# Performance work log

Measured on AMD Instinct MI355X. Metric: run time of the kernel, lower is better.

The kernel has to match this reference:

```python
import jax, jax.numpy as jnp
import numpy as np

T = 524288
INPUT_LEN = 64
N_MEMORY = 64
OUTPUT_LEN = 32


def setup_inputs() -> dict:
    key = jax.random.key(0)
    k_x, k_w1, k_b1, k_w2, k_b2 = jax.random.split(key, 5)
    s = 0.05  # tf.random_normal_initializer default stddev
    return {
        "inputs": jax.random.normal(k_x, (T, INPUT_LEN), dtype=jnp.float32),
        "W1": s * jax.random.normal(k_w1, (INPUT_LEN, 2 * N_MEMORY), dtype=jnp.float32),
        "B1": s * jax.random.normal(k_b1, (1, 2 * N_MEMORY), dtype=jnp.float32),
        "W2": s * jax.random.normal(k_w2, (N_MEMORY, OUTPUT_LEN), dtype=jnp.float32),
        "B2": s * jax.random.normal(k_b2, (1, OUTPUT_LEN), dtype=jnp.float32),
    }


def reference(inputs, W1, B1, W2, B2):
    n_memory = W2.shape[0]
    # gates: h = sigmoid(x W1 + B1), split into left/right halves  [T, M] each
    h = jax.nn.sigmoid(inputs @ W1 + B1)
    left, right = jnp.split(h, 2, axis=1)
    prod = left * right
    # affine linear recurrence: u_t = prod_{t-1} * u_{t-1} + (1 - left_{t-1}), u_0 = 0
    a = prod[:-1]            # [T-1, M] multiplicative coeffs
    b = 1.0 - left[:-1]      # [T-1, M] additive terms

    def step(u, ab):
        a_t, b_t = ab
        u = a_t * u + b_t
        return u, u

    u0 = jnp.zeros((n_memory,), dtype=inputs.dtype)
    _, us = jax.lax.scan(step, u0, (a, b))
    z = jnp.concatenate([u0[None, :], us], axis=0)  # [T, M]
    out = z @ W2 + B2                               # [T, output_len]
    return out
```

## Files before the change

kernel.cpp:

```cpp
#include <hip/hip_runtime.h>

#define TT    524288
#define CHUNK 512
#define NCH   (TT / CHUNK)
#define SUB   64
#define NSUB  (CHUNK / SUB)

typedef __attribute__((ext_vector_type(8))) short short8;
typedef __attribute__((ext_vector_type(4))) float f32x4;

__device__ __forceinline__ unsigned short f2bf(float f) {
    union { float f; unsigned u; } v; v.f = f;
    unsigned r = v.u + 0x7FFFu + ((v.u >> 16) & 1u);
    return (unsigned short)(r >> 16);
}
__device__ __forceinline__ unsigned packbf2(float a, float b) {
    union { float f; unsigned u; } va, vb; va.f = a; vb.f = b;
    unsigned ra = va.u + 0x7FFFu + ((va.u >> 16) & 1u);
    unsigned rb = vb.u + 0x7FFFu + ((vb.u >> 16) & 1u);
    return (ra >> 16) | (rb & 0xFFFF0000u);
}
__device__ __forceinline__ float2 unpackbf2(unsigned w) {
    union { unsigned u; float f; } a, b;
    a.u = w << 16; b.u = w & 0xFFFF0000u;
    return make_float2(a.f, b.f);
}
__device__ __forceinline__ float sigf(float v) {
    return __builtin_amdgcn_rcpf(1.0f + __expf(-v));
}

template <bool EMIT>
__global__ __launch_bounds__(256, 3)
void dphase(const float* __restrict__ x, const float* __restrict__ W1,
            const float* __restrict__ B1, const float* __restrict__ W2,
            const float* __restrict__ B2, const float* __restrict__ carry,
            float* __restrict__ Aout, float* __restrict__ Bout,
            float* __restrict__ out)
{
    __shared__ __align__(16) short    W1t[128 * 72];
    __shared__ float    B1s[128];
    __shared__ __align__(16) short    XZ[SUB * 72];
    __shared__ unsigned abp[SUB * 65];
    __shared__ float    segA[4 * 66], segB[4 * 66];
    __shared__ float    ucur[64];
    __shared__ __align__(16) short    W2t[32 * 72];
    __shared__ float    B2s[32];

    const int tid  = threadIdx.x;
    const int c    = blockIdx.x;
    const int wave = tid >> 6;
    const int lane = tid & 63;
    const int quad = lane >> 4;
    const int lr   = lane & 15;

    for (int i = tid; i < 2048; i += 256) {
        float4 w4 = ((const float4*)W1)[i];
        int k = i >> 5, n0 = (i & 31) * 4;
        W1t[(n0 + 0) * 72 + k] = (short)f2bf(w4.x);
        W1t[(n0 + 1) * 72 + k] = (short)f2bf(w4.y);
        W1t[(n0 + 2) * 72 + k] = (short)f2bf(w4.z);
        W1t[(n0 + 3) * 72 + k] = (short)f2bf(w4.w);
    }
    if (tid < 128) B1s[tid] = B1[tid];
    if (EMIT) {
        for (int i = tid; i < 512; i += 256) {
            float4 w4 = ((const float4*)W2)[i];
            int k = i >> 3, n0 = (i & 7) * 4;
            W2t[(n0 + 0) * 72 + k] = (short)f2bf(w4.x);
            W2t[(n0 + 1) * 72 + k] = (short)f2bf(w4.y);
            W2t[(n0 + 2) * 72 + k] = (short)f2bf(w4.z);
            W2t[(n0 + 3) * 72 + k] = (short)f2bf(w4.w);
        }
        if (tid < 32) B2s[tid] = B2[tid];
        if (tid < 64) ucur[tid] = carry[c * 64 + tid];
    }

    const float4* xg = (const float4*)(x + (size_t)c * CHUNK * 64);
    float4 xr0 = xg[tid], xr1 = xg[tid + 256], xr2 = xg[tid + 512], xr3 = xg[tid + 768];

    float sA = 1.0f, sB = 0.0f;

    for (int s = 0; s < NSUB; ++s) {
        {
            float4 v; int f;
#define PUTX(R, J) { v = (R); f = tid + 256 * (J); int row = f >> 4, c4 = (f & 15) * 4; \
            unsigned lo = (unsigned)f2bf(v.x) | ((unsigned)f2bf(v.y) << 16); \
            unsigned hi = (unsigned)f2bf(v.z) | ((unsigned)f2bf(v.w) << 16); \
            *(uint2*)&XZ[row * 72 + c4] = make_uint2(lo, hi); }
            PUTX(xr0, 0) PUTX(xr1, 1) PUTX(xr2, 2) PUTX(xr3, 3)
#undef PUTX
        }
        __syncthreads();

        if (s + 1 < NSUB) {
            const float4* xn = xg + (size_t)(s + 1) * 1024;
            xr0 = xn[tid]; xr1 = xn[tid + 256]; xr2 = xn[tid + 512]; xr3 = xn[tid + 768];
        }

        f32x4 acc[8];
        #pragma unroll
        for (int j = 0; j < 8; ++j) {
            float b = B1s[j * 16 + lr];
            acc[j][0] = b; acc[j][1] = b; acc[j][2] = b; acc[j][3] = b;
        }
        const short8 a0 = *(const short8*)&XZ[(wave * 16 + lr) * 72 + quad * 8];
        const short8 a1 = *(const short8*)&XZ[(wave * 16 + lr) * 72 + quad * 8 + 32];
        #pragma unroll
        for (int j = 0; j < 8; ++j) {
            const short8 b0 = *(const short8*)&W1t[(j * 16 + lr) * 72 + quad * 8];
            const short8 b1 = *(const short8*)&W1t[(j * 16 + lr) * 72 + quad * 8 + 32];
            acc[j] = __builtin_amdgcn_mfma_f32_16x16x32_bf16(a0, b0, acc[j], 0, 0, 0);
            acc[j] = __builtin_amdgcn_mfma_f32_16x16x32_bf16(a1, b1, acc[j], 0, 0, 0);
        }

        #pragma unroll
        for (int j = 0; j < 4; ++j) {
            #pragma unroll
            for (int r = 0; r < 4; ++r) {
                float hl = sigf(acc[j][r]);
                float hr = sigf(acc[j + 4][r]);
                int m = wave * 16 + quad * 4 + r;
                abp[m * 65 + j * 16 + lr] = packbf2(hl * hr, 1.0f - hl);
            }
        }
        __syncthreads();

        float A = 1.0f, Bv = 0.0f;
        #pragma unroll
        for (int t = 0; t < 16; ++t) {
            float2 f2 = unpackbf2(abp[(wave * 16 + t) * 65 + lane]);
            Bv = fmaf(f2.x, Bv, f2.y); A *= f2.x;
        }
        segA[wave * 66 + lane] = A;
        segB[wave * 66 + lane] = Bv;
        __syncthreads();

        if (EMIT) {
            float u = ucur[lane];
            #pragma unroll
            for (int q = 0; q < 3; ++q)
                if (q < wave) u = fmaf(segA[q * 66 + lane], u, segB[q * 66 + lane]);
            #pragma unroll
            for (int t = 0; t < 16; ++t) {
                float2 f2 = unpackbf2(abp[(wave * 16 + t) * 65 + lane]);
                XZ[(wave * 16 + t) * 72 + lane] = (short)f2bf(u);
                u = fmaf(f2.x, u, f2.y);
            }
            if (wave == 3) ucur[lane] = u;

            const short8 za0 = *(const short8*)&XZ[(wave * 16 + lr) * 72 + quad * 8];
            const short8 za1 = *(const short8*)&XZ[(wave * 16 + lr) * 72 + quad * 8 + 32];
            const size_t row0g = (size_t)c * CHUNK + (size_t)s * SUB;
            #pragma unroll
            for (int nt = 0; nt < 2; ++nt) {
                f32x4 cc;
                float b = B2s[nt * 16 + lr];
                cc[0] = b; cc[1] = b; cc[2] = b; cc[3] = b;
                const short8 b0 = *(const short8*)&W2t[(nt * 16 + lr) * 72 + quad * 8];
                const short8 b1 = *(const short8*)&W2t[(nt * 16 + lr) * 72 + quad * 8 + 32];
                cc = __builtin_amdgcn_mfma_f32_16x16x32_bf16(za0, b0, cc, 0, 0, 0);
                cc = __builtin_amdgcn_mfma_f32_16x16x32_bf16(za1, b1, cc, 0, 0, 0);
                #pragma unroll
                for (int r = 0; r < 4; ++r) {
                    int m = wave * 16 + quad * 4 + r;
                    out[(row0g + m) * 32 + nt * 16 + lr] = cc[r];
                }
            }
            __syncthreads();
        } else {
            if (tid < 64) {
                #pragma unroll
                for (int q = 0; q < 4; ++q) {
                    float A2 = segA[q * 66 + tid], B2v = segB[q * 66 + tid];
                    sB = fmaf(A2, sB, B2v); sA *= A2;
                }
            }
        }
    }

    if (!EMIT && tid < 64) { Aout[c * 64 + tid] = sA; Bout[c * 64 + tid] = sB; }
}

__global__ void carry_scan(const float* __restrict__ Aar, const float* __restrict__ Bar,
                           float* __restrict__ carry)
{
    __shared__ float sA[16 * 66], sB[16 * 66];
    const int tid = threadIdx.x;
    const int ch = tid & 63, seg = tid >> 6;
    const int c0 = seg * (NCH / 16);

    float A = 1.0f, B = 0.0f;
    #pragma unroll 8
    for (int i = 0; i < NCH / 16; ++i) {
        const int idx = c0 + i;
        const float a = Aar[idx * 64 + ch];
        const float b = Bar[idx * 64 + ch];
        B = fmaf(a, B, b); A *= a;
    }
    sA[seg * 66 + ch] = A;
    sB[seg * 66 + ch] = B;
    __syncthreads();

    float u = 0.0f;
    #pragma unroll
    for (int q = 0; q < 15; ++q)
        if (q < seg) u = fmaf(sA[q * 66 + ch], u, sB[q * 66 + ch]);
    #pragma unroll 8
    for (int i = 0; i < NCH / 16; ++i) {
        const int idx = c0 + i;
        carry[idx * 64 + ch] = u;
        u = fmaf(Aar[idx * 64 + ch], u, Bar[idx * 64 + ch]);
    }
}

extern "C" void kernel_launch(void* const* d_in, const int* in_sizes, int n_in,
                              void* d_out, int out_size, void* d_ws, size_t ws_size,
                              hipStream_t stream)
{
    const float* x  = (const float*)d_in[0];
    const float* W1 = (const float*)d_in[1];
    const float* B1 = (const float*)d_in[2];
    const float* W2 = (const float*)d_in[3];
    const float* B2 = (const float*)d_in[4];
    float* out = (float*)d_out;

    float* Aar   = (float*)d_ws;
    float* Bar   = Aar + NCH * 64;
    float* carry = Bar + NCH * 64;

    dphase<false><<<NCH, 256, 0, stream>>>(x, W1, B1, W2, B2, nullptr,
                                           Aar, Bar, nullptr);
    carry_scan<<<1, 1024, 0, stream>>>(Aar, Bar, carry);
    dphase<true><<<NCH, 256, 0, stream>>>(x, W1, B1, W2, B2, carry,
                                          nullptr, nullptr, out);
}
```

Baseline: 301.7 us.

## Store gate coefficients in phase one and drop recompute in emit phase

```diff
diff --git a/kernel.cpp b/kernel.cpp
--- a/kernel.cpp
+++ b/kernel.cpp
@@ -29,22 +29,17 @@
     return __builtin_amdgcn_rcpf(1.0f + __expf(-v));
 }
 
-template <bool EMIT>
 __global__ __launch_bounds__(256, 3)
-void dphase(const float* __restrict__ x, const float* __restrict__ W1,
-            const float* __restrict__ B1, const float* __restrict__ W2,
-            const float* __restrict__ B2, const float* __restrict__ carry,
+void aphase(const float* __restrict__ x, const float* __restrict__ W1,
+            const float* __restrict__ B1,
             float* __restrict__ Aout, float* __restrict__ Bout,
-            float* __restrict__ out)
+            uint4* __restrict__ abg)
 {
     __shared__ __align__(16) short    W1t[128 * 72];
     __shared__ float    B1s[128];
     __shared__ __align__(16) short    XZ[SUB * 72];
     __shared__ unsigned abp[SUB * 65];
     __shared__ float    segA[4 * 66], segB[4 * 66];
-    __shared__ float    ucur[64];
-    __shared__ __align__(16) short    W2t[32 * 72];
-    __shared__ float    B2s[32];
 
     const int tid  = threadIdx.x;
     const int c    = blockIdx.x;
@@ -62,18 +57,6 @@
         W1t[(n0 + 3) * 72 + k] = (short)f2bf(w4.w);
     }
     if (tid < 128) B1s[tid] = B1[tid];
-    if (EMIT) {
-        for (int i = tid; i < 512; i += 256) {
-            float4 w4 = ((const float4*)W2)[i];
-            int k = i >> 3, n0 = (i & 7) * 4;
-            W2t[(n0 + 0) * 72 + k] = (short)f2bf(w4.x);
-            W2t[(n0 + 1) * 72 + k] = (short)f2bf(w4.y);
-            W2t[(n0 + 2) * 72 + k] = (short)f2bf(w4.z);
-            W2t[(n0 + 3) * 72 + k] = (short)f2bf(w4.w);
-        }
-        if (tid < 32) B2s[tid] = B2[tid];
-        if (tid < 64) ucur[tid] = carry[c * 64 + tid];
-    }
 
     const float4* xg = (const float4*)(x + (size_t)c * CHUNK * 64);
     float4 xr0 = xg[tid], xr1 = xg[tid + 256], xr2 = xg[tid + 512], xr3 = xg[tid + 768];
@@ -125,6 +108,19 @@
         }
         __syncthreads();
 
+        {
+            uint4* dst = abg + ((size_t)((c * NSUB + s) * 16 + wave * 4)) * 64 + lane;
+            #pragma unroll
+            for (int i = 0; i < 4; ++i) {
+                uint4 v;
+                v.x = abp[(wave * 16 + i * 4 + 0) * 65 + lane];
+                v.y = abp[(wave * 16 + i * 4 + 1) * 65 + lane];
+                v.z = abp[(wave * 16 + i * 4 + 2) * 65 + lane];
+                v.w = abp[(wave * 16 + i * 4 + 3) * 65 + lane];
+                dst[i * 64] = v;
+            }
+        }
+
         float A = 1.0f, Bv = 0.0f;
         #pragma unroll
         for (int t = 0; t < 16; ++t) {
@@ -135,50 +131,16 @@
         segB[wave * 66 + lane] = Bv;
         __syncthreads();
 
-        if (EMIT) {
-            float u = ucur[lane];
-            #pragma unroll
-            for (int q = 0; q < 3; ++q)
-                if (q < wave) u = fmaf(segA[q * 66 + lane], u, segB[q * 66 + lane]);
-            #pragma unroll
-            for (int t = 0; t < 16; ++t) {
-                float2 f2 = unpackbf2(abp[(wave * 16 + t) * 65 + lane]);
-                XZ[(wave * 16 + t) * 72 + lane] = (short)f2bf(u);
-                u = fmaf(f2.x, u, f2.y);
-            }
-            if (wave == 3) ucur[lane] = u;
-
-            const short8 za0 = *(const short8*)&XZ[(wave * 16 + lr) * 72 + quad * 8];
-            const short8 za1 = *(const short8*)&XZ[(wave * 16 + lr) * 72 + quad * 8 + 32];
-            const size_t row0g = (size_t)c * CHUNK + (size_t)s * SUB;
-            #pragma unroll
-            for (int nt = 0; nt < 2; ++nt) {
-                f32x4 cc;
-                float b = B2s[nt * 16 + lr];
-                cc[0] = b; cc[1] = b; cc[2] = b; cc[3] = b;
-                const short8 b0 = *(const short8*)&W2t[(nt * 16 + lr) * 72 + quad * 8];
-                const short8 b1 = *(const short8*)&W2t[(nt * 16 + lr) * 72 + quad * 8 + 32];
-                cc = __builtin_amdgcn_mfma_f32_16x16x32_bf16(za0, b0, cc, 0, 0, 0);
-                cc = __builtin_amdgcn_mfma_f32_16x16x32_bf16(za1, b1, cc, 0, 0, 0);
-                #pragma unroll
-                for (int r = 0; r < 4; ++r) {
-                    int m = wave * 16 + quad * 4 + r;
-                    out[(row0g + m) * 32 + nt * 16 + lr] = cc[r];
-                }
-            }
-            __syncthreads();
-        } else {
-            if (tid < 64) {
-                #pragma unroll
-                for (int q = 0; q < 4; ++q) {
-                    float A2 = segA[q * 66 + tid], B2v = segB[q * 66 + tid];
-                    sB = fmaf(A2, sB, B2v); sA *= A2;
-                }
-            }
-        }
-    }
-
-    if (!EMIT && tid < 64) { Aout[c * 64 + tid] = sA; Bout[c * 64 + tid] = sB; }
+        if (tid < 64) {
+            #pragma unroll
+            for (int q = 0; q < 4; ++q) {
+                float A2 = segA[q * 66 + tid], B2v = segB[q * 66 + tid];
+                sB = fmaf(A2, sB, B2v); sA *= A2;
+            }
+        }
+    }
+
+    if (tid < 64) { Aout[c * 64 + tid] = sA; Bout[c * 64 + tid] = sB; }
 }
 
 __global__ void carry_scan(const float* __restrict__ Aar, const float* __restrict__ Bar,
@@ -213,6 +175,98 @@
     }
 }
 
+__global__ __launch_bounds__(256, 4)
+void ephase(const uint4* __restrict__ abg, const float* __restrict__ carry,
+            const float* __restrict__ W2, const float* __restrict__ B2,
+            float* __restrict__ out)
+{
+    __shared__ __align__(16) short Zs[SUB * 72];
+    __shared__ float segA[2 * 4 * 66], segB[2 * 4 * 66];
+    __shared__ __align__(16) short W2t[32 * 72];
+    __shared__ float B2s[32];
+    __shared__ float ucur[2 * 64];
+
+    const int tid  = threadIdx.x;
+    const int c    = blockIdx.x;
+    const int wave = tid >> 6;
+    const int lane = tid & 63;
+    const int quad = lane >> 4;
+    const int lr   = lane & 15;
+
+    for (int i = tid; i < 512; i += 256) {
+        float4 w4 = ((const float4*)W2)[i];
+        int k = i >> 3, n0 = (i & 7) * 4;
+        W2t[(n0 + 0) * 72 + k] = (short)f2bf(w4.x);
+        W2t[(n0 + 1) * 72 + k] = (short)f2bf(w4.y);
+        W2t[(n0 + 2) * 72 + k] = (short)f2bf(w4.z);
+        W2t[(n0 + 3) * 72 + k] = (short)f2bf(w4.w);
+    }
+    if (tid < 32) B2s[tid] = B2[tid];
+    if (tid < 64) ucur[tid] = carry[c * 64 + tid];
+
+    const uint4* ag = abg + (size_t)c * (NSUB * 16 * 64);
+    uint4 r0 = ag[(wave * 4 + 0) * 64 + lane];
+    uint4 r1 = ag[(wave * 4 + 1) * 64 + lane];
+    uint4 r2 = ag[(wave * 4 + 2) * 64 + lane];
+    uint4 r3 = ag[(wave * 4 + 3) * 64 + lane];
+
+    for (int s = 0; s < NSUB; ++s) {
+        const int pb = (s & 1) * 264;
+        float A = 1.0f, Bv = 0.0f; float2 f;
+#define CSTEP(W) { f = unpackbf2(W); Bv = fmaf(f.x, Bv, f.y); A *= f.x; }
+        CSTEP(r0.x) CSTEP(r0.y) CSTEP(r0.z) CSTEP(r0.w)
+        CSTEP(r1.x) CSTEP(r1.y) CSTEP(r1.z) CSTEP(r1.w)
+        CSTEP(r2.x) CSTEP(r2.y) CSTEP(r2.z) CSTEP(r2.w)
+        CSTEP(r3.x) CSTEP(r3.y) CSTEP(r3.z) CSTEP(r3.w)
+#undef CSTEP
+        segA[pb + wave * 66 + lane] = A;
+        segB[pb + wave * 66 + lane] = Bv;
+        __syncthreads();
+
+        float u = ucur[(s & 1) * 64 + lane];
+        #pragma unroll
+        for (int q = 0; q < 3; ++q)
+            if (q < wave) u = fmaf(segA[pb + q * 66 + lane], u, segB[pb + q * 66 + lane]);
+
+        int t = 0;
+#define ESTEP(W) { Zs[(wave * 16 + t) * 72 + lane] = (short)f2bf(u); \
+                   f = unpackbf2(W); u = fmaf(f.x, u, f.y); ++t; }
+        ESTEP(r0.x) ESTEP(r0.y) ESTEP(r0.z) ESTEP(r0.w)
+        ESTEP(r1.x) ESTEP(r1.y) ESTEP(r1.z) ESTEP(r1.w)
+        ESTEP(r2.x) ESTEP(r2.y) ESTEP(r2.z) ESTEP(r2.w)
+        ESTEP(r3.x) ESTEP(r3.y) ESTEP(r3.z) ESTEP(r3.w)
+#undef ESTEP
+        if (wave == 3) ucur[((s + 1) & 1) * 64 + lane] = u;
+
+        if (s + 1 < NSUB) {
+            const uint4* an = ag + (size_t)(s + 1) * (16 * 64);
+            r0 = an[(wave * 4 + 0) * 64 + lane];
+            r1 = an[(wave * 4 + 1) * 64 + lane];
+            r2 = an[(wave * 4 + 2) * 64 + lane];
+            r3 = an[(wave * 4 + 3) * 64 + lane];
+        }
+
+        const short8 za0 = *(const short8*)&Zs[(wave * 16 + lr) * 72 + quad * 8];
+        const short8 za1 = *(const short8*)&Zs[(wave * 16 + lr) * 72 + quad * 8 + 32];
+        const size_t row0g = (size_t)c * CHUNK + (size_t)s * SUB;
+        #pragma unroll
+        for (int nt = 0; nt < 2; ++nt) {
+            f32x4 cc;
+            float b = B2s[nt * 16 + lr];
+            cc[0] = b; cc[1] = b; cc[2] = b; cc[3] = b;
+            const short8 b0 = *(const short8*)&W2t[(nt * 16 + lr) * 72 + quad * 8];
+            const short8 b1 = *(const short8*)&W2t[(nt * 16 + lr) * 72 + quad * 8 + 32];
+            cc = __builtin_amdgcn_mfma_f32_16x16x32_bf16(za0, b0, cc, 0, 0, 0);
+            cc = __builtin_amdgcn_mfma_f32_16x16x32_bf16(za1, b1, cc, 0, 0, 0);
+            #pragma unroll
+            for (int r = 0; r < 4; ++r) {
+                int m = wave * 16 + quad * 4 + r;
+                out[(row0g + m) * 32 + nt * 16 + lr] = cc[r];
+            }
+        }
+    }
+}
+
 extern "C" void kernel_launch(void* const* d_in, const int* in_sizes, int n_in,
                               void* d_out, int out_size, void* d_ws, size_t ws_size,
                               hipStream_t stream)
@@ -227,10 +281,9 @@
     float* Aar   = (float*)d_ws;
     float* Bar   = Aar + NCH * 64;
     float* carry = Bar + NCH * 64;
-
-    dphase<false><<<NCH, 256, 0, stream>>>(x, W1, B1, W2, B2, nullptr,
-                                           Aar, Bar, nullptr);
+    uint4* abg   = (uint4*)(carry + NCH * 64);
+
+    aphase<<<NCH, 256, 0, stream>>>(x, W1, B1, Aar, Bar, abg);
     carry_scan<<<1, 1024, 0, stream>>>(Aar, Bar, carry);
-    dphase<true><<<NCH, 256, 0, stream>>>(x, W1, B1, W2, B2, carry,
-                                          nullptr, nullptr, out);
-}
+    ephase<<<NCH, 256, 0, stream>>>(abg, carry, W2, B2, out);
+}
```

New measurement: 302.3 us. No clear change (+0.2%).
